# Optimization experiments

Measured on AMD Instinct MI355X. Metric: run time of the kernel, lower is better.

The kernel has to match this reference:

```python
import jax, jax.numpy as jnp
import numpy as np

N = 100_000      # nodes
E = 3_200_000    # edges (avg degree 32)
F = 16           # irrep feature channels
IR = 4           # (max_l+1)**2 with max_l = 1
DENOM = 32.0     # denominator init kwarg
EPS = 1e-9
INV_S3 = 1.0 / np.sqrt(3.0).astype(np.float32)  # CG norm for 1x1->0
INV_S2 = 1.0 / np.sqrt(2.0).astype(np.float32)  # CG norm for 1x1->1


def setup_inputs() -> dict:
    key = jax.random.key(0)
    k0, k1, k2, k3, k4 = jax.random.split(key, 5)
    positions = jax.random.normal(k0, (N, 3), jnp.float32)
    node_feats = jax.random.normal(k1, (N, F, IR), jnp.float32)
    W = jax.random.normal(k2, (IR, IR), jnp.float32) / np.float32(np.sqrt(IR))
    b = jnp.zeros((IR,), jnp.float32)
    senders = jax.random.randint(k3, (E,), 0, N)
    receivers = jax.random.randint(k4, (E,), 0, N)
    return dict(positions=positions, node_feats=node_feats, W=W, b=b,
                senders=senders, receivers=receivers)


def reference(positions, node_feats, W, b, senders, receivers):
    # --- edge update: SH of normalized relative position, CG tensor product ---
    d = positions[receivers] - positions[senders]               # [E, 3]
    d = d / (jnp.linalg.norm(d, axis=-1, keepdims=True) + EPS)  # unit direction
    # real spherical harmonics up to l=1: sh0 = 1, sh1 = unit direction
    sh1 = d[:, None, :]                                         # [E, 1, 3]

    x = node_feats[senders]                                     # [E, F, 4]
    x0 = x[..., 0:1]                                            # l=0 part [E,F,1]
    x1 = x[..., 1:4]                                            # l=1 part [E,F,3]

    # CG paths with l3 <= max_l = 1:
    #   0x0->0 (identity), 1x1->0 (dot / sqrt3)
    out0 = x0 + jnp.sum(x1 * sh1, axis=-1, keepdims=True) * INV_S3      # [E,F,1]
    #   0x1->1, 1x0->1 (identities), 1x1->1 (cross / sqrt2)
    cross = jnp.cross(x1, jnp.broadcast_to(sh1, x1.shape))
    out1 = x0 * sh1 + x1 + cross * INV_S2                               # [E,F,3]
    tp = jnp.concatenate([out0, out1], axis=-1)                         # [E,F,4]

    # --- node update: segment-sum over receivers, scale, Dense over coeff dim ---
    agg = jax.ops.segment_sum(tp, receivers, num_segments=positions.shape[0])
    agg = agg / DENOM                                                   # [N,F,4]
    return agg @ W + b                                                  # [N,F,4]
```

## Files before the change

kernel.cpp:

```cpp
#include <hip/hip_runtime.h>


#define F_DIM 16
#define BIN_SHIFT 6
#define BIN_NODES (1 << BIN_SHIFT)
#define CHUNK 8192
#define STG (CHUNK / 256)
#define CAP_LDS 2816

__global__ void __launch_bounds__(256) init_kernel(int* __restrict__ binCur,
                                                   int nbins, int cap)
{
    int b = blockIdx.x * blockDim.x + threadIdx.x;
    if (b < nbins) binCur[b] = b * cap;
}

__global__ void __launch_bounds__(256) pos_pack_kernel(
    const float* __restrict__ pos, float4* __restrict__ posf4, int N)
{
    int n = blockIdx.x * blockDim.x + threadIdx.x;
    if (n >= N) return;
    posf4[n] = make_float4(pos[3*n], pos[3*n+1], pos[3*n+2], 0.f);
}

__global__ void __launch_bounds__(256) build_bins_kernel(
    const int* __restrict__ senders, const int* __restrict__ receivers,
    int* __restrict__ binCur, int* __restrict__ bins,
    int nbins, int cap, int E)
{
    __shared__ int hist[2048];
    int t = threadIdx.x;
    for (int i = t; i < nbins; i += 256) hist[i] = 0;
    __syncthreads();

    int base = blockIdx.x * CHUNK;
    unsigned pk[STG], br[STG];
#pragma unroll
    for (int k = 0; k < STG; ++k) {
        int e = base + k * 256 + t;
        if (e < E) {
            int r = receivers[e];
            int s = senders[e];
            int bb = r >> BIN_SHIFT;
            int rank = atomicAdd(&hist[bb], 1);
            pk[k] = ((unsigned)s << BIN_SHIFT) | (unsigned)(r & (BIN_NODES - 1));
            br[k] = ((unsigned)bb << 13) | (unsigned)rank;
        } else {
            br[k] = 0xFFFFFFFFu;
        }
    }
    __syncthreads();

    for (int i = t; i < nbins; i += 256) {
        int c = hist[i];
        if (c > 0) hist[i] = atomicAdd(&binCur[i], c);
    }
    __syncthreads();

#pragma unroll
    for (int k = 0; k < STG; ++k) {
        if (br[k] == 0xFFFFFFFFu) continue;
        int bb   = (int)(br[k] >> 13);
        int rank = (int)(br[k] & 8191u);
        int dest = hist[bb] + rank;
        if (dest < (bb + 1) * cap)
            bins[dest] = (int)pk[k];
    }
}

__device__ __forceinline__ void edge_acc(
    const float4& pr, const float4& sp, const float4& fx,
    float& a0, float& a1, float& a2, float& a3)
{
    const float INV_S3 = 0.5773502691896258f;
    const float INV_S2 = 0.7071067811865476f;
    float dx = pr.x - sp.x;
    float dy = pr.y - sp.y;
    float dz = pr.z - sp.z;
    float d2 = dx*dx + dy*dy + dz*dz;
    float inv = __builtin_amdgcn_rsqf(fmaxf(d2, 1e-18f));
    dx *= inv; dy *= inv; dz *= inv;
    float dot = fx.y*dx + fx.z*dy + fx.w*dz;
    a0 += fx.x + dot * INV_S3;
    float c0 = fx.z*dz - fx.w*dy;
    float c1 = fx.w*dx - fx.y*dz;
    float c2 = fx.y*dy - fx.z*dx;
    a1 += fx.x*dx + fx.y + c0 * INV_S2;
    a2 += fx.x*dy + fx.z + c1 * INV_S2;
    a3 += fx.x*dz + fx.w + c2 * INV_S2;
}

__global__ void __launch_bounds__(256) bin_gather_kernel(
    const float4* __restrict__ posf4,
    const float* __restrict__ nf,
    const int* __restrict__ bins,
    const int* __restrict__ binCur,
    const float* __restrict__ W,
    const float* __restrict__ Bias,
    float* __restrict__ out,
    int N, int cap)
{
    __shared__ int lcsr[CAP_LDS];
    __shared__ int lhist[BIN_NODES];
    __shared__ int lscan[BIN_NODES];
    __shared__ int lstart[BIN_NODES];

    int t = threadIdx.x;
    int bin = blockIdx.x;
    int node0 = bin << BIN_SHIFT;
    int gbase = bin * cap;

    int cnt = binCur[bin] - gbase;
    if (cnt > cap) cnt = cap;

    if (t < BIN_NODES) lhist[t] = 0;
    __syncthreads();

    for (int j = t; j < cnt; j += 256)
        atomicAdd(&lhist[((unsigned)bins[gbase + j]) & (BIN_NODES - 1)], 1);
    __syncthreads();

    if (t < BIN_NODES) lscan[t] = lhist[t];
    __syncthreads();
    for (int off = 1; off < BIN_NODES; off <<= 1) {
        int v = (t < BIN_NODES && t >= off) ? lscan[t - off] : 0;
        __syncthreads();
        if (t < BIN_NODES) lscan[t] += v;
        __syncthreads();
    }
    if (t < BIN_NODES) { lstart[t] = lscan[t] - lhist[t]; lhist[t] = 0; }
    __syncthreads();

    for (int j = t; j < cnt; j += 256) {
        unsigned pk = (unsigned)bins[gbase + j];
        int rl = (int)(pk & (BIN_NODES - 1));
        int rank = atomicAdd(&lhist[rl], 1);
        lcsr[lstart[rl] + rank] = (int)(pk >> BIN_SHIFT);
    }
    __syncthreads();

    float w[16];
#pragma unroll
    for (int i = 0; i < 16; ++i) w[i] = W[i];
    float b0 = Bias[0], b1 = Bias[1], b2 = Bias[2], b3 = Bias[3];
    const float sc = 1.0f / 32.0f;

    int f = t & 15;
    const float4* nf4 = (const float4*)nf;

    for (int nl = t >> 4; nl < BIN_NODES; nl += 16) {
        int n = node0 + nl;
        if (n >= N) break;
        float4 pr = posf4[n];
        int s0 = lstart[nl];
        int dcnt = lscan[nl] - s0;

        float a0 = 0.f, a1 = 0.f, a2 = 0.f, a3 = 0.f;
        int j = 0;
        for (; j + 4 <= dcnt; j += 4) {
            int s_0 = lcsr[s0 + j + 0];
            int s_1 = lcsr[s0 + j + 1];
            int s_2 = lcsr[s0 + j + 2];
            int s_3 = lcsr[s0 + j + 3];
            float4 p0 = posf4[s_0];
            float4 p1 = posf4[s_1];
            float4 p2 = posf4[s_2];
            float4 p3 = posf4[s_3];
            float4 q0 = nf4[(unsigned)(s_0 * F_DIM + f)];
            float4 q1 = nf4[(unsigned)(s_1 * F_DIM + f)];
            float4 q2 = nf4[(unsigned)(s_2 * F_DIM + f)];
            float4 q3 = nf4[(unsigned)(s_3 * F_DIM + f)];
            edge_acc(pr, p0, q0, a0, a1, a2, a3);
            edge_acc(pr, p1, q1, a0, a1, a2, a3);
            edge_acc(pr, p2, q2, a0, a1, a2, a3);
            edge_acc(pr, p3, q3, a0, a1, a2, a3);
        }
        for (; j < dcnt; ++j) {
            int s = lcsr[s0 + j];
            float4 p = posf4[s];
            float4 q = nf4[(unsigned)(s * F_DIM + f)];
            edge_acc(pr, p, q, a0, a1, a2, a3);
        }

        a0 *= sc; a1 *= sc; a2 *= sc; a3 *= sc;
        float4 o;
        o.x = a0*w[0] + a1*w[4] + a2*w[8]  + a3*w[12] + b0;
        o.y = a0*w[1] + a1*w[5] + a2*w[9]  + a3*w[13] + b1;
        o.z = a0*w[2] + a1*w[6] + a2*w[10] + a3*w[14] + b2;
        o.w = a0*w[3] + a1*w[7] + a2*w[11] + a3*w[15] + b3;
        ((float4*)out)[(size_t)n * F_DIM + f] = o;
    }
}

__global__ void __launch_bounds__(256) hist_kernel(
    const int* __restrict__ receivers, int* __restrict__ deg,
    int* __restrict__ rank, int E)
{
    int e = blockIdx.x * blockDim.x + threadIdx.x;
    if (e >= E) return;
    rank[e] = atomicAdd(&deg[receivers[e]], 1);
}

__global__ void __launch_bounds__(256) alloc_kernel(
    const int* __restrict__ deg, int* __restrict__ start,
    int* __restrict__ cursor, int N)
{
    __shared__ int tmp[256];
    __shared__ int base;
    int t = threadIdx.x;
    int n = blockIdx.x * blockDim.x + t;
    int v = (n < N) ? deg[n] : 0;
    tmp[t] = v;
    __syncthreads();
    for (int off = 1; off < 256; off <<= 1) {
        int x = (t >= off) ? tmp[t - off] : 0;
        __syncthreads();
        tmp[t] += x;
        __syncthreads();
    }
    int incl = tmp[t];
    if (t == 255) base = atomicAdd(cursor, incl);
    __syncthreads();
    if (n < N) start[n] = base + incl - v;
}

__global__ void __launch_bounds__(256) scatter_kernel(
    const int* __restrict__ senders, const int* __restrict__ receivers,
    const int* __restrict__ rank, const int* __restrict__ start,
    int* __restrict__ csr_s, int E)
{
    int e = blockIdx.x * blockDim.x + threadIdx.x;
    if (e >= E) return;
    csr_s[start[receivers[e]] + rank[e]] = senders[e];
}

__global__ void __launch_bounds__(256) gather_kernel(
    const float* __restrict__ pos,
    const float* __restrict__ nf,
    const int* __restrict__ csr_s,
    const int* __restrict__ start,
    const int* __restrict__ deg,
    const float* __restrict__ W,
    const float* __restrict__ b,
    float* __restrict__ out,
    int N)
{
    const float INV_S3 = 0.5773502691896258f;
    const float INV_S2 = 0.7071067811865476f;

    int tid = blockIdx.x * blockDim.x + threadIdx.x;
    int n = tid >> 4;
    if (n >= N) return;
    int f = tid & 15;

    float rx = pos[3*n], ry = pos[3*n+1], rz = pos[3*n+2];
    int s0 = start[n];
    int dcnt = deg[n];
    float a0 = 0.f, a1 = 0.f, a2 = 0.f, a3 = 0.f;
    const float4* nf4 = (const float4*)nf;

    int s = (dcnt > 0) ? csr_s[s0] : 0;
    for (int j = 0; j < dcnt; ++j) {
        int s_next = (j + 1 < dcnt) ? csr_s[s0 + j + 1] : 0;
        float dx = rx - pos[3*s], dy = ry - pos[3*s+1], dz = rz - pos[3*s+2];
        float d2 = dx*dx + dy*dy + dz*dz;
        float inv = __builtin_amdgcn_rsqf(fmaxf(d2, 1e-18f));
        dx *= inv; dy *= inv; dz *= inv;
        float4 x = nf4[(unsigned)(s * F_DIM + f)];
        float x0 = x.x, x1 = x.y, x2 = x.z, x3 = x.w;
        float dot = x1*dx + x2*dy + x3*dz;
        a0 += x0 + dot * INV_S3;
        float c0 = x2*dz - x3*dy, c1 = x3*dx - x1*dz, c2 = x1*dy - x2*dx;
        a1 += x0*dx + x1 + c0 * INV_S2;
        a2 += x0*dy + x2 + c1 * INV_S2;
        a3 += x0*dz + x3 + c2 * INV_S2;
        s = s_next;
    }
    const float sc = 1.0f / 32.0f;
    a0 *= sc; a1 *= sc; a2 *= sc; a3 *= sc;
    float4 o;
    o.x = a0*W[0] + a1*W[4] + a2*W[8]  + a3*W[12] + b[0];
    o.y = a0*W[1] + a1*W[5] + a2*W[9]  + a3*W[13] + b[1];
    o.z = a0*W[2] + a1*W[6] + a2*W[10] + a3*W[14] + b[2];
    o.w = a0*W[3] + a1*W[7] + a2*W[11] + a3*W[15] + b[3];
    ((float4*)out)[tid] = o;
}

extern "C" void kernel_launch(void* const* d_in, const int* in_sizes, int n_in,
                              void* d_out, int out_size, void* d_ws, size_t ws_size,
                              hipStream_t stream)
{
    const float* pos       = (const float*)d_in[0];
    const float* nf        = (const float*)d_in[1];
    const float* W         = (const float*)d_in[2];
    const float* b         = (const float*)d_in[3];
    const int*   senders   = (const int*)d_in[4];
    const int*   receivers = (const int*)d_in[5];

    int N = in_sizes[0] / 3;
    int E = in_sizes[4];
    float* out = (float*)d_out;
    const int blk = 256;

    int nbins = (N + BIN_NODES - 1) >> BIN_SHIFT;
    int cap   = E / nbins + 453;
    size_t need = ((size_t)N * 4 + (size_t)nbins * cap + nbins) * sizeof(float);

    if (nbins <= 2048 && cap <= CAP_LDS && ws_size >= need) {
        float4* posf4 = (float4*)d_ws;
        int* binCur = (int*)(posf4 + N);
        int* bins   = binCur + nbins;

        pos_pack_kernel<<<(N + blk - 1) / blk, blk, 0, stream>>>(pos, posf4, N);
        init_kernel<<<(nbins + blk - 1) / blk, blk, 0, stream>>>(binCur, nbins, cap);
        build_bins_kernel<<<(E + CHUNK - 1) / CHUNK, blk, 0, stream>>>(
            senders, receivers, binCur, bins, nbins, cap, E);
        bin_gather_kernel<<<nbins, blk, 0, stream>>>(
            posf4, nf, bins, binCur, W, b, out, N, cap);
    } else {
        int* cursor = (int*)d_ws;
        int* deg    = cursor + 1;
        int* start  = deg + N;
        int* rank   = start + N;
        int* csr_s  = rank + E;

        hipMemsetAsync(cursor, 0, (size_t)(1 + N) * sizeof(int), stream);
        hist_kernel<<<(E + blk - 1) / blk, blk, 0, stream>>>(receivers, deg, rank, E);
        alloc_kernel<<<(N + blk - 1) / blk, blk, 0, stream>>>(deg, start, cursor, N);
        scatter_kernel<<<(E + blk - 1) / blk, blk, 0, stream>>>(
            senders, receivers, rank, start, csr_s, E);
        long total = (long)N * F_DIM;
        gather_kernel<<<(unsigned)((total + blk - 1) / blk), blk, 0, stream>>>(
            pos, nf, csr_s, start, deg, W, b, out, N);
    }
}
```

Before: 279.1 us.

## Use smaller bins, two-pass binning with few blocks, and deeper gather unroll

Result: slower. 442.8 us (+58.7%).

```diff
diff --git a/kernel.cpp b/kernel.cpp
--- a/kernel.cpp
+++ b/kernel.cpp
@@ -2,69 +2,55 @@
 
 
 #define F_DIM 16
-#define BIN_SHIFT 6
+#define BIN_SHIFT 5
 #define BIN_NODES (1 << BIN_SHIFT)
-#define CHUNK 8192
-#define STG (CHUNK / 256)
-#define CAP_LDS 2816
-
-__global__ void __launch_bounds__(256) init_kernel(int* __restrict__ binCur,
-                                                   int nbins, int cap)
-{
-    int b = blockIdx.x * blockDim.x + threadIdx.x;
-    if (b < nbins) binCur[b] = b * cap;
-}
-
-__global__ void __launch_bounds__(256) pos_pack_kernel(
-    const float* __restrict__ pos, float4* __restrict__ posf4, int N)
-{
-    int n = blockIdx.x * blockDim.x + threadIdx.x;
-    if (n >= N) return;
-    posf4[n] = make_float4(pos[3*n], pos[3*n+1], pos[3*n+2], 0.f);
-}
-
-__global__ void __launch_bounds__(256) build_bins_kernel(
+#define GBLK 128
+#define CAP_LDS 1344
+#define MAX_BINS 3584
+#define BUILD_BLOCKS 64
+
+__global__ void __launch_bounds__(256) setup_kernel(
+    const float* __restrict__ pos, float4* __restrict__ posf4,
+    int* __restrict__ binCur, int N, int nbins, int cap)
+{
+    int i = blockIdx.x * blockDim.x + threadIdx.x;
+    if (i < N) posf4[i] = make_float4(pos[3*i], pos[3*i+1], pos[3*i+2], 0.f);
+    if (i < nbins) binCur[i] = i * cap;
+}
+
+__global__ void __launch_bounds__(256) build2_kernel(
     const int* __restrict__ senders, const int* __restrict__ receivers,
     int* __restrict__ binCur, int* __restrict__ bins,
     int nbins, int cap, int E)
 {
-    __shared__ int hist[2048];
+    __shared__ int hbase[MAX_BINS];
+    __shared__ int hcnt[MAX_BINS];
     int t = threadIdx.x;
-    for (int i = t; i < nbins; i += 256) hist[i] = 0;
-    __syncthreads();
-
-    int base = blockIdx.x * CHUNK;
-    unsigned pk[STG], br[STG];
-#pragma unroll
-    for (int k = 0; k < STG; ++k) {
-        int e = base + k * 256 + t;
-        if (e < E) {
-            int r = receivers[e];
-            int s = senders[e];
-            int bb = r >> BIN_SHIFT;
-            int rank = atomicAdd(&hist[bb], 1);
-            pk[k] = ((unsigned)s << BIN_SHIFT) | (unsigned)(r & (BIN_NODES - 1));
-            br[k] = ((unsigned)bb << 13) | (unsigned)rank;
-        } else {
-            br[k] = 0xFFFFFFFFu;
-        }
-    }
+    for (int i = t; i < nbins; i += 256) hcnt[i] = 0;
+    __syncthreads();
+
+    int chunk = (E + gridDim.x - 1) / gridDim.x;
+    int e0 = blockIdx.x * chunk;
+    int e1 = min(e0 + chunk, E);
+
+    for (int e = e0 + t; e < e1; e += 256)
+        atomicAdd(&hcnt[receivers[e] >> BIN_SHIFT], 1);
     __syncthreads();
 
     for (int i = t; i < nbins; i += 256) {
-        int c = hist[i];
-        if (c > 0) hist[i] = atomicAdd(&binCur[i], c);
-    }
-    __syncthreads();
-
-#pragma unroll
-    for (int k = 0; k < STG; ++k) {
-        if (br[k] == 0xFFFFFFFFu) continue;
-        int bb   = (int)(br[k] >> 13);
-        int rank = (int)(br[k] & 8191u);
-        int dest = hist[bb] + rank;
+        int c = hcnt[i];
+        hbase[i] = (c > 0) ? atomicAdd(&binCur[i], c) : 0;
+        hcnt[i] = 0;
+    }
+    __syncthreads();
+
+    for (int e = e0 + t; e < e1; e += 256) {
+        int r = receivers[e];
+        int bb = r >> BIN_SHIFT;
+        int k = atomicAdd(&hcnt[bb], 1);
+        int dest = hbase[bb] + k;
         if (dest < (bb + 1) * cap)
-            bins[dest] = (int)pk[k];
+            bins[dest] = (senders[e] << BIN_SHIFT) | (r & (BIN_NODES - 1));
     }
 }
 
@@ -90,7 +76,7 @@
     a3 += fx.x*dz + fx.w + c2 * INV_S2;
 }
 
-__global__ void __launch_bounds__(256) bin_gather_kernel(
+__global__ void __launch_bounds__(GBLK) bin_gather_kernel(
     const float4* __restrict__ posf4,
     const float* __restrict__ nf,
     const int* __restrict__ bins,
@@ -116,8 +102,8 @@
     if (t < BIN_NODES) lhist[t] = 0;
     __syncthreads();
 
-    for (int j = t; j < cnt; j += 256)
-        atomicAdd(&lhist[((unsigned)bins[gbase + j]) & (BIN_NODES - 1)], 1);
+    for (int j = t; j < cnt; j += GBLK)
+        atomicAdd(&lhist[bins[gbase + j] & (BIN_NODES - 1)], 1);
     __syncthreads();
 
     if (t < BIN_NODES) lscan[t] = lhist[t];
@@ -131,24 +117,19 @@
     if (t < BIN_NODES) { lstart[t] = lscan[t] - lhist[t]; lhist[t] = 0; }
     __syncthreads();
 
-    for (int j = t; j < cnt; j += 256) {
-        unsigned pk = (unsigned)bins[gbase + j];
-        int rl = (int)(pk & (BIN_NODES - 1));
-        int rank = atomicAdd(&lhist[rl], 1);
-        lcsr[lstart[rl] + rank] = (int)(pk >> BIN_SHIFT);
-    }
-    __syncthreads();
-
-    float w[16];
-#pragma unroll
-    for (int i = 0; i < 16; ++i) w[i] = W[i];
-    float b0 = Bias[0], b1 = Bias[1], b2 = Bias[2], b3 = Bias[3];
-    const float sc = 1.0f / 32.0f;
+    for (int j = t; j < cnt; j += GBLK) {
+        int pk = bins[gbase + j];
+        int rl = pk & (BIN_NODES - 1);
+        int k = atomicAdd(&lhist[rl], 1);
+        lcsr[lstart[rl] + k] = pk >> BIN_SHIFT;
+    }
+    __syncthreads();
 
     int f = t & 15;
     const float4* nf4 = (const float4*)nf;
-
-    for (int nl = t >> 4; nl < BIN_NODES; nl += 16) {
+    const float sc = 1.0f / 32.0f;
+
+    for (int nl = t >> 4; nl < BIN_NODES; nl += GBLK / 16) {
         int n = node0 + nl;
         if (n >= N) break;
         float4 pr = posf4[n];
@@ -157,23 +138,19 @@
 
         float a0 = 0.f, a1 = 0.f, a2 = 0.f, a3 = 0.f;
         int j = 0;
-        for (; j + 4 <= dcnt; j += 4) {
-            int s_0 = lcsr[s0 + j + 0];
-            int s_1 = lcsr[s0 + j + 1];
-            int s_2 = lcsr[s0 + j + 2];
-            int s_3 = lcsr[s0 + j + 3];
-            float4 p0 = posf4[s_0];
-            float4 p1 = posf4[s_1];
-            float4 p2 = posf4[s_2];
-            float4 p3 = posf4[s_3];
-            float4 q0 = nf4[(unsigned)(s_0 * F_DIM + f)];
-            float4 q1 = nf4[(unsigned)(s_1 * F_DIM + f)];
-            float4 q2 = nf4[(unsigned)(s_2 * F_DIM + f)];
-            float4 q3 = nf4[(unsigned)(s_3 * F_DIM + f)];
-            edge_acc(pr, p0, q0, a0, a1, a2, a3);
-            edge_acc(pr, p1, q1, a0, a1, a2, a3);
-            edge_acc(pr, p2, q2, a0, a1, a2, a3);
-            edge_acc(pr, p3, q3, a0, a1, a2, a3);
+        for (; j + 8 <= dcnt; j += 8) {
+            int ss[8];
+            float4 p[8], q[8];
+#pragma unroll
+            for (int k = 0; k < 8; ++k) ss[k] = lcsr[s0 + j + k];
+#pragma unroll
+            for (int k = 0; k < 8; ++k) {
+                p[k] = posf4[ss[k]];
+                q[k] = nf4[(unsigned)(ss[k] * F_DIM + f)];
+            }
+#pragma unroll
+            for (int k = 0; k < 8; ++k)
+                edge_acc(pr, p[k], q[k], a0, a1, a2, a3);
         }
         for (; j < dcnt; ++j) {
             int s = lcsr[s0 + j];
@@ -184,10 +161,10 @@
 
         a0 *= sc; a1 *= sc; a2 *= sc; a3 *= sc;
         float4 o;
-        o.x = a0*w[0] + a1*w[4] + a2*w[8]  + a3*w[12] + b0;
-        o.y = a0*w[1] + a1*w[5] + a2*w[9]  + a3*w[13] + b1;
-        o.z = a0*w[2] + a1*w[6] + a2*w[10] + a3*w[14] + b2;
-        o.w = a0*w[3] + a1*w[7] + a2*w[11] + a3*w[15] + b3;
+        o.x = a0*W[0] + a1*W[4] + a2*W[8]  + a3*W[12] + Bias[0];
+        o.y = a0*W[1] + a1*W[5] + a2*W[9]  + a3*W[13] + Bias[1];
+        o.z = a0*W[2] + a1*W[6] + a2*W[10] + a3*W[14] + Bias[2];
+        o.w = a0*W[3] + a1*W[7] + a2*W[11] + a3*W[15] + Bias[3];
         ((float4*)out)[(size_t)n * F_DIM + f] = o;
     }
 }
@@ -303,19 +280,20 @@
     const int blk = 256;
 
     int nbins = (N + BIN_NODES - 1) >> BIN_SHIFT;
-    int cap   = E / nbins + 453;
+    int cap   = E / nbins + 320;
     size_t need = ((size_t)N * 4 + (size_t)nbins * cap + nbins) * sizeof(float);
 
-    if (nbins <= 2048 && cap <= CAP_LDS && ws_size >= need) {
+    if (nbins <= MAX_BINS && cap <= CAP_LDS && ws_size >= need) {
         float4* posf4 = (float4*)d_ws;
         int* binCur = (int*)(posf4 + N);
         int* bins   = binCur + nbins;
 
-        pos_pack_kernel<<<(N + blk - 1) / blk, blk, 0, stream>>>(pos, posf4, N);
-        init_kernel<<<(nbins + blk - 1) / blk, blk, 0, stream>>>(binCur, nbins, cap);
-        build_bins_kernel<<<(E + CHUNK - 1) / CHUNK, blk, 0, stream>>>(
+        int setup_n = (N > nbins ? N : nbins);
+        setup_kernel<<<(setup_n + blk - 1) / blk, blk, 0, stream>>>(
+            pos, posf4, binCur, N, nbins, cap);
+        build2_kernel<<<BUILD_BLOCKS, blk, 0, stream>>>(
             senders, receivers, binCur, bins, nbins, cap, E);
-        bin_gather_kernel<<<nbins, blk, 0, stream>>>(
+        bin_gather_kernel<<<nbins, GBLK, 0, stream>>>(
             posf4, nf, bins, binCur, W, b, out, N, cap);
     } else {
         int* cursor = (int*)d_ws;
```

## Replace single-pass binning with two-level coarse/fine radix partition

Applied to the files above, without the earlier changes.

New measurement: 302.5 us. 1.08x slower.

```diff
diff --git a/kernel.cpp b/kernel.cpp
--- a/kernel.cpp
+++ b/kernel.cpp
@@ -4,67 +4,99 @@
 #define F_DIM 16
 #define BIN_SHIFT 6
 #define BIN_NODES (1 << BIN_SHIFT)
-#define CHUNK 8192
-#define STG (CHUNK / 256)
+#define C_SHIFT 11
+#define FPB (1 << (C_SHIFT - BIN_SHIFT))
 #define CAP_LDS 2816
-
-__global__ void __launch_bounds__(256) init_kernel(int* __restrict__ binCur,
-                                                   int nbins, int cap)
-{
-    int b = blockIdx.x * blockDim.x + threadIdx.x;
-    if (b < nbins) binCur[b] = b * cap;
-}
-
-__global__ void __launch_bounds__(256) pos_pack_kernel(
-    const float* __restrict__ pos, float4* __restrict__ posf4, int N)
-{
-    int n = blockIdx.x * blockDim.x + threadIdx.x;
-    if (n >= N) return;
-    posf4[n] = make_float4(pos[3*n], pos[3*n+1], pos[3*n+2], 0.f);
-}
-
-__global__ void __launch_bounds__(256) build_bins_kernel(
+#define MAXB1 512
+#define BPB 32
+
+__global__ void __launch_bounds__(256) setup_kernel(
+    const float* __restrict__ pos, float4* __restrict__ posf4,
+    int* __restrict__ binCur, int* __restrict__ bucketCur,
+    int N, int nbins, int cap, int NB1, int cap1)
+{
+    int i = blockIdx.x * blockDim.x + threadIdx.x;
+    if (i < N) posf4[i] = make_float4(pos[3*i], pos[3*i+1], pos[3*i+2], 0.f);
+    if (i < nbins) binCur[i] = i * cap;
+    if (i < NB1) bucketCur[i] = i * cap1;
+}
+
+__global__ void __launch_bounds__(256) coarse_kernel(
     const int* __restrict__ senders, const int* __restrict__ receivers,
+    int* __restrict__ bucketCur, int* __restrict__ bucketA,
+    int NB1, int cap1, int E)
+{
+    __shared__ int hbase[MAXB1];
+    __shared__ int hcnt[MAXB1];
+    int t = threadIdx.x;
+    for (int i = t; i < NB1; i += 256) hcnt[i] = 0;
+    __syncthreads();
+
+    int chunk = (E + gridDim.x - 1) / gridDim.x;
+    int e0 = blockIdx.x * chunk;
+    int e1 = min(e0 + chunk, E);
+
+    for (int e = e0 + t; e < e1; e += 256)
+        atomicAdd(&hcnt[receivers[e] >> C_SHIFT], 1);
+    __syncthreads();
+
+    for (int i = t; i < NB1; i += 256) {
+        int c = hcnt[i];
+        hbase[i] = (c > 0) ? atomicAdd(&bucketCur[i], c) : 0;
+        hcnt[i] = 0;
+    }
+    __syncthreads();
+
+    for (int e = e0 + t; e < e1; e += 256) {
+        int r = receivers[e];
+        int b = r >> C_SHIFT;
+        int k = atomicAdd(&hcnt[b], 1);
+        int dest = hbase[b] + k;
+        if (dest < (b + 1) * cap1)
+            bucketA[dest] = (senders[e] << C_SHIFT) | (r & ((1 << C_SHIFT) - 1));
+    }
+}
+
+__global__ void __launch_bounds__(256) fine_kernel(
+    const int* __restrict__ bucketA, const int* __restrict__ bucketCur,
     int* __restrict__ binCur, int* __restrict__ bins,
-    int nbins, int cap, int E)
-{
-    __shared__ int hist[2048];
+    int cap1, int cap)
+{
+    __shared__ int hb[FPB];
+    __shared__ int hc[FPB];
     int t = threadIdx.x;
-    for (int i = t; i < nbins; i += 256) hist[i] = 0;
-    __syncthreads();
-
-    int base = blockIdx.x * CHUNK;
-    unsigned pk[STG], br[STG];
-#pragma unroll
-    for (int k = 0; k < STG; ++k) {
-        int e = base + k * 256 + t;
-        if (e < E) {
-            int r = receivers[e];
-            int s = senders[e];
-            int bb = r >> BIN_SHIFT;
-            int rank = atomicAdd(&hist[bb], 1);
-            pk[k] = ((unsigned)s << BIN_SHIFT) | (unsigned)(r & (BIN_NODES - 1));
-            br[k] = ((unsigned)bb << 13) | (unsigned)rank;
-        } else {
-            br[k] = 0xFFFFFFFFu;
-        }
-    }
-    __syncthreads();
-
-    for (int i = t; i < nbins; i += 256) {
-        int c = hist[i];
-        if (c > 0) hist[i] = atomicAdd(&binCur[i], c);
-    }
-    __syncthreads();
-
-#pragma unroll
-    for (int k = 0; k < STG; ++k) {
-        if (br[k] == 0xFFFFFFFFu) continue;
-        int bb   = (int)(br[k] >> 13);
-        int rank = (int)(br[k] & 8191u);
-        int dest = hist[bb] + rank;
-        if (dest < (bb + 1) * cap)
-            bins[dest] = (int)pk[k];
+    int bucket = blockIdx.x / BPB;
+    int bi     = blockIdx.x % BPB;
+
+    int cnt = bucketCur[bucket] - bucket * cap1;
+    if (cnt > cap1) cnt = cap1;
+    int lo = (int)((long)cnt * bi / BPB);
+    int hi = (int)((long)cnt * (bi + 1) / BPB);
+    int base = bucket * cap1;
+
+    if (t < FPB) hc[t] = 0;
+    __syncthreads();
+
+    for (int j = lo + t; j < hi; j += 256)
+        atomicAdd(&hc[(bucketA[base + j] >> BIN_SHIFT) & (FPB - 1)], 1);
+    __syncthreads();
+
+    if (t < FPB) {
+        int c = hc[t];
+        int gb = (bucket << (C_SHIFT - BIN_SHIFT)) + t;
+        hb[t] = (c > 0) ? atomicAdd(&binCur[gb], c) : 0;
+        hc[t] = 0;
+    }
+    __syncthreads();
+
+    for (int j = lo + t; j < hi; j += 256) {
+        int u = bucketA[base + j];
+        int lb = (u >> BIN_SHIFT) & (FPB - 1);
+        int k = atomicAdd(&hc[lb], 1);
+        int dest = hb[lb] + k;
+        int gb = (bucket << (C_SHIFT - BIN_SHIFT)) + lb;
+        if (dest < (gb + 1) * cap)
+            bins[dest] = ((u >> C_SHIFT) << BIN_SHIFT) | (u & (BIN_NODES - 1));
     }
 }
 
@@ -117,7 +149,7 @@
     __syncthreads();
 
     for (int j = t; j < cnt; j += 256)
-        atomicAdd(&lhist[((unsigned)bins[gbase + j]) & (BIN_NODES - 1)], 1);
+        atomicAdd(&lhist[bins[gbase + j] & (BIN_NODES - 1)], 1);
     __syncthreads();
 
     if (t < BIN_NODES) lscan[t] = lhist[t];
@@ -132,10 +164,10 @@
     __syncthreads();
 
     for (int j = t; j < cnt; j += 256) {
-        unsigned pk = (unsigned)bins[gbase + j];
-        int rl = (int)(pk & (BIN_NODES - 1));
-        int rank = atomicAdd(&lhist[rl], 1);
-        lcsr[lstart[rl] + rank] = (int)(pk >> BIN_SHIFT);
+        int pk = bins[gbase + j];
+        int rl = pk & (BIN_NODES - 1);
+        int k = atomicAdd(&lhist[rl], 1);
+        lcsr[lstart[rl] + k] = pk >> BIN_SHIFT;
     }
     __syncthreads();
 
@@ -304,17 +336,28 @@
 
     int nbins = (N + BIN_NODES - 1) >> BIN_SHIFT;
     int cap   = E / nbins + 453;
-    size_t need = ((size_t)N * 4 + (size_t)nbins * cap + nbins) * sizeof(float);
-
-    if (nbins <= 2048 && cap <= CAP_LDS && ws_size >= need) {
-        float4* posf4 = (float4*)d_ws;
-        int* binCur = (int*)(posf4 + N);
-        int* bins   = binCur + nbins;
-
-        pos_pack_kernel<<<(N + blk - 1) / blk, blk, 0, stream>>>(pos, posf4, N);
-        init_kernel<<<(nbins + blk - 1) / blk, blk, 0, stream>>>(binCur, nbins, cap);
-        build_bins_kernel<<<(E + CHUNK - 1) / CHUNK, blk, 0, stream>>>(
-            senders, receivers, binCur, bins, nbins, cap, E);
+    int NB1   = (N + (1 << C_SHIFT) - 1) >> C_SHIFT;
+    int cap1  = (int)((long)E * (1 << C_SHIFT) / N + 4096);
+
+    size_t need = (size_t)N * 16 +
+                  ((size_t)nbins + NB1 + (size_t)NB1 * cap1 + (size_t)nbins * cap) * 4;
+
+    bool pack_ok = (N <= (1 << (31 - C_SHIFT)));
+
+    if (nbins >= 1 && NB1 <= MAXB1 && cap <= CAP_LDS && pack_ok && ws_size >= need) {
+        float4* posf4    = (float4*)d_ws;
+        int* binCur      = (int*)(posf4 + N);
+        int* bucketCur   = binCur + nbins;
+        int* bucketA     = bucketCur + NB1;
+        int* bins        = bucketA + (size_t)NB1 * cap1;
+
+        int setup_n = N > nbins ? N : nbins;
+        setup_kernel<<<(setup_n + blk - 1) / blk, blk, 0, stream>>>(
+            pos, posf4, binCur, bucketCur, N, nbins, cap, NB1, cap1);
+        coarse_kernel<<<256, blk, 0, stream>>>(
+            senders, receivers, bucketCur, bucketA, NB1, cap1, E);
+        fine_kernel<<<NB1 * BPB, blk, 0, stream>>>(
+            bucketA, bucketCur, binCur, bins, cap1, cap);
         bin_gather_kernel<<<nbins, blk, 0, stream>>>(
             posf4, nf, bins, binCur, W, b, out, N, cap);
     } else {
```
